# Kernel optimization log

Hardware: AMD Instinct MI355X
Metric: run time of the kernel (lower is better)

## Reference

```python
import jax, jax.numpy as jnp
import numpy as np

B, T, N, C = 16, 12, 2048, 64
WIN = 3                    # window_size
F = 3                      # len(filters) branches
NW = T - WIN + 1           # number of windows = 10


def setup_inputs() -> dict:
    key = jax.random.key(0)
    k0, k1, k2, k3, k4 = jax.random.split(key, 5)
    data = jax.random.normal(k0, (B, T, N, C), jnp.float32)
    # scale adj so aggregated features stay O(1)
    adj = jax.random.normal(k1, (WIN * N, WIN * N), jnp.float32) / np.float32(np.sqrt(WIN * N))
    temporal_emb = jax.random.normal(k2, (1, T, 1, C), jnp.float32) * 0.1
    spatial_emb = jax.random.normal(k3, (1, 1, N, C), jnp.float32) * 0.1
    # per-window, per-filter GLU linear: C -> 2C
    W = jax.random.normal(k4, (NW, F, C, 2 * C), jnp.float32) / np.float32(np.sqrt(C))
    b = jnp.zeros((NW, F, 2 * C), jnp.float32)
    return {"data": data, "adj": adj, "temporal_emb": temporal_emb,
            "spatial_emb": spatial_emb, "W": W, "b": b}


def reference(data, adj, temporal_emb, spatial_emb, W, b):
    # data: (B,T,N,C); adj: (3N,3N)
    x = data + temporal_emb + spatial_emb                     # (B,T,N,C)
    # sliding windows of 3 time steps, flattened to 3N nodes  # (B,NW,3N,C)
    wins = jnp.stack([x[:, i:i + WIN].reshape(B, WIN * N, C) for i in range(NW)], axis=1)
    # only the middle N rows of the bmm output survive the mid-step slice,
    # so aggregate with just those rows of adj (same math, less work)
    adj_mid = adj[(WIN - 1) // 2 * N:(WIN + 1) // 2 * N]      # (N, 3N)
    agg = jnp.einsum('mn,bwnc->bwmc', adj_mid, wins)          # (B,NW,N,C)
    # per-window per-filter linear C -> 2C, then GLU
    pre = jnp.einsum('bwnc,wfcd->bwfnd', agg, W) + b[None, :, :, None, :]  # (B,NW,F,N,2C)
    lhs, rhs = jnp.split(pre, 2, axis=-1)
    glu = lhs * jax.nn.sigmoid(rhs)                           # (B,NW,F,N,C)
    # max over filter branches -> (B, T-2, N, C)
    return jnp.max(glu, axis=2)
```

## Files before the change

kernel.cpp:

```cpp
#include <hip/hip_runtime.h>
#include <hip/hip_bf16.h>

#define B_ 16
#define T_ 12
#define N_ 2048
#define C_ 64
#define NW_ 10
#define K_ 6144

#define NT32 192
#define ALDS32 4096
#define BLDS32 10240

typedef __attribute__((ext_vector_type(8))) short bf16x8;
typedef __attribute__((ext_vector_type(4))) float f32x4;

__device__ __forceinline__ unsigned short f2bf(float f) {
  union { float f; unsigned int u; } v; v.f = f;
  unsigned int u = v.u;
  return (unsigned short)((u + 0x7FFFu + ((u >> 16) & 1u)) >> 16);
}

__device__ __forceinline__ void gload16(const void* g, void* l) {
  __builtin_amdgcn_global_load_lds(
      (const __attribute__((address_space(1))) unsigned int*)g,
      (__attribute__((address_space(3))) unsigned int*)l, 16, 0, 0);
}

template<int N>
__device__ __forceinline__ void vmw() {
  if constexpr (N == 5) asm volatile("s_waitcnt vmcnt(5)" ::: "memory");
  else                  asm volatile("s_waitcnt vmcnt(0)" ::: "memory");
}

__global__ __launch_bounds__(256) void prep_x2(const float* __restrict__ data,
                                               const float* __restrict__ temb,
                                               const float* __restrict__ semb,
                                               unsigned short* __restrict__ xbt2) {
  int idx = blockIdx.x * 256 + threadIdx.x;
  int q = idx & 511;
  int btnb = idx >> 9;
  int nb = btnb & 31;
  int bt = btnb >> 5;
  int t = bt % T_;
  int o = q >> 6, c = q & 63;
  int n0 = nb * 64 + o * 8;
  float te = temb[t * C_ + c];
  union { unsigned short s[8]; uint4 v; } pk;
#pragma unroll
  for (int e = 0; e < 8; ++e) {
    int n = n0 + e;
    float d = data[((size_t)bt * N_ + n) * C_ + c];
    float se = semb[(size_t)n * C_ + c];
    pk.s[e] = f2bf(d + te + se);
  }
  *(uint4*)(xbt2 + (size_t)idx * 8) = pk.v;
}

__global__ __launch_bounds__(256) void prep_adj3(const float* __restrict__ adj,
                                                 unsigned short* __restrict__ adjb3) {
  int idx = blockIdx.x * 256 + threadIdx.x;
  int s = idx & 63;
  int l4 = s >> 4, l15 = s & 15;
  int chunk = idx >> 6;
  int rg = chunk & 7;
  int KK = (chunk >> 3) & 1;
  int tb = chunk >> 4;
  int t = tb % 96;
  int bmt = tb / 96;
  int m = bmt * 128 + rg * 16 + l15;
  int k = t * 64 + KK * 32 + l4 * 8;
  const float* src = adj + ((size_t)(N_ + m)) * K_ + k;
  float4 a = *(const float4*)src;
  float4 b4 = *(const float4*)(src + 4);
  union { unsigned short s8[8]; uint4 v; } pk;
  pk.s8[0] = f2bf(a.x);  pk.s8[1] = f2bf(a.y);  pk.s8[2] = f2bf(a.z);  pk.s8[3] = f2bf(a.w);
  pk.s8[4] = f2bf(b4.x); pk.s8[5] = f2bf(b4.y); pk.s8[6] = f2bf(b4.z); pk.s8[7] = f2bf(b4.w);
  *(uint4*)(adjb3 + (size_t)idx * 8) = pk.v;
}

__global__ __launch_bounds__(256) void prep_w(const float* __restrict__ W,
                                              unsigned short* __restrict__ wbt) {
  int idx = blockIdx.x * 256 + threadIdx.x;
  int c = idx & 63;
  int d = (idx >> 6) & 127;
  int wf = idx >> 13;
  float v = W[((size_t)wf * 64 + c) * 128 + d];
  wbt[idx] = f2bf(v);
}

struct SegCtx {
  const unsigned short* Asrc;
  const unsigned short* Xroot;
  int lane, wid, wid5, l4, l15, fbase;
  int bconst[5];
};

template<int UA, int UB3>
__device__ __forceinline__ void phase32(const SegCtx& s, unsigned short* ldsA,
                                        unsigned short* ldsB, int u, f32x4 (&acc)[8][5]) {
  if (u + 1 < NT32) {
    const unsigned short* As = s.Asrc + (size_t)(u + 1) * 4096;
    unsigned short* Ad = ldsA + (UA ^ 1) * ALDS32;
#pragma unroll
    for (int ci = 0; ci < 2; ++ci) {
      int rg = s.wid * 2 + ci;
      gload16(As + rg * 512 + s.lane * 8, Ad + rg * 512);
    }
  }
  if (u + 2 < NT32) {
    const unsigned short* Bs = s.Xroot + (size_t)(u + 2) * 2048;
    unsigned short* Bd = ldsB + ((UB3 + 2) % 3) * BLDS32;
#pragma unroll
    for (int ci = 0; ci < 5; ++ci) {
      int cg = s.wid5 + ci;
      gload16(Bs + s.bconst[ci], Bd + cg * 512);
    }
  }
  const unsigned short* Ab = ldsA + UA * ALDS32;
  const unsigned short* Bb = ldsB + UB3 * BLDS32;
  bf16x8 af[8], bfv[5];
#pragma unroll
  for (int c = 0; c < 5; ++c)
    bfv[c] = *(const bf16x8*)(Bb + (s.wid5 + c) * 512 + s.fbase);
#pragma unroll
  for (int i = 0; i < 8; ++i)
    af[i] = *(const bf16x8*)(Ab + i * 512 + s.fbase);
  __builtin_amdgcn_s_setprio(1);
#pragma unroll
  for (int i = 0; i < 8; ++i)
#pragma unroll
    for (int c = 0; c < 5; ++c)
      acc[i][c] = __builtin_amdgcn_mfma_f32_16x16x32_bf16(af[i], bfv[c], acc[i][c], 0, 0, 0);
  __builtin_amdgcn_s_setprio(0);
  if (u < NT32 - 2) vmw<5>();
  else if (u == NT32 - 2) vmw<0>();
  if (u < NT32 - 1) {
    __builtin_amdgcn_s_barrier();
    __builtin_amdgcn_sched_barrier(0);
  }
}

__global__ __launch_bounds__(256, 2) void gemm_agg(const unsigned short* __restrict__ adjb3,
                                                   const unsigned short* __restrict__ xbt2,
                                                   unsigned short* __restrict__ aggb) {
  __shared__ __align__(16) unsigned short ldsA[2 * ALDS32];
  __shared__ __align__(16) unsigned short ldsB[3 * BLDS32];
  int bid = blockIdx.x;
  int bmt = bid & 15;
  int bs = bid >> 4;
  int b = bs >> 1;
  int w0 = (bs & 1) * 5;
  int tid = threadIdx.x;
  SegCtx s;
  s.lane = tid & 63; s.wid = tid >> 6;
  s.wid5 = s.wid * 5;
  s.l4 = s.lane >> 4; s.l15 = s.lane & 15;
  s.fbase = s.l4 * 128 + s.l15 * 8;
  s.Asrc = adjb3 + (size_t)bmt * 786432;
  s.Xroot = xbt2 + ((size_t)(b * T_ + w0)) * C_ * N_;
  int bOffLane = s.l4 * 512 + s.l15 * 8;
#pragma unroll
  for (int ci = 0; ci < 5; ++ci) {
    int cg = s.wid5 + ci;
    s.bconst[ci] = (cg >> 2) * 131072 + (cg & 3) * 128 + bOffLane;
  }

  f32x4 acc[8][5];
#pragma unroll
  for (int i = 0; i < 8; ++i)
#pragma unroll
    for (int c = 0; c < 5; ++c) acc[i][c] = (f32x4)0.f;

  __builtin_amdgcn_sched_barrier(0);
#pragma unroll
  for (int ci = 0; ci < 2; ++ci) {
    int rg = s.wid * 2 + ci;
    gload16(s.Asrc + rg * 512 + s.lane * 8, ldsA + rg * 512);
  }
#pragma unroll
  for (int ci = 0; ci < 5; ++ci)
    gload16(s.Xroot + s.bconst[ci], ldsB + (s.wid5 + ci) * 512);
#pragma unroll
  for (int ci = 0; ci < 5; ++ci)
    gload16(s.Xroot + 2048 + s.bconst[ci], ldsB + BLDS32 + (s.wid5 + ci) * 512);
  vmw<5>();
  __builtin_amdgcn_s_barrier();
  __builtin_amdgcn_sched_barrier(0);

  for (int it = 0; it < NT32 / 6; ++it) {
    int u = it * 6;
    phase32<0, 0>(s, ldsA, ldsB, u,     acc);
    phase32<1, 1>(s, ldsA, ldsB, u + 1, acc);
    phase32<0, 2>(s, ldsA, ldsB, u + 2, acc);
    phase32<1, 0>(s, ldsA, ldsB, u + 3, acc);
    phase32<0, 1>(s, ldsA, ldsB, u + 4, acc);
    phase32<1, 2>(s, ldsA, ldsB, u + 5, acc);
  }

  unsigned short* Ob0 = aggb + (size_t)(b * NW_ + w0) * N_ * C_;
#pragma unroll
  for (int c = 0; c < 5; ++c) {
    int col = s.wid * 80 + c * 16 + s.l15;
    int g = col >> 6, cc = col & 63;
    unsigned short* Ob = Ob0 + (size_t)g * N_ * C_ + cc;
#pragma unroll
    for (int i = 0; i < 8; ++i) {
      int n0 = bmt * 128 + i * 16 + s.l4 * 4;
#pragma unroll
      for (int q = 0; q < 4; ++q)
        Ob[(size_t)(n0 + q) * C_] = f2bf(acc[i][c][q]);
    }
  }
}

__global__ __launch_bounds__(256) void glu_out(const unsigned short* __restrict__ aggb,
                                               const unsigned short* __restrict__ wbt,
                                               const float* __restrict__ bias,
                                               float* __restrict__ out) {
  __shared__ __align__(16) unsigned short sW[3 * 128 * 64];
  int bn = blockIdx.x, bw = blockIdx.y;
  int w = bw % NW_;
  int tid = threadIdx.x, lane = tid & 63, wid = tid >> 6;
  int lrow8 = lane >> 3, jl = lane & 7;
  int l15 = lane & 15, l4 = lane >> 4;
  const unsigned short* Wsrc = wbt + (size_t)w * 3 * 128 * 64;
  for (int ci = 0; ci < 12; ++ci) {
    int chunk = wid * 12 + ci;
    int row = chunk * 8 + lrow8;
    int jg = jl ^ (row & 7);
    gload16(Wsrc + (size_t)row * 64 + jg * 8, &sW[chunk * 512]);
  }
  const unsigned short* Abase = aggb + ((size_t)bw * N_ + bn * 128 + wid * 32) * C_;
  bf16x8 af[2][2];
  for (int i = 0; i < 2; ++i)
    for (int kh = 0; kh < 2; ++kh)
      af[i][kh] = *(const bf16x8*)(Abase + (size_t)(i * 16 + l15) * C_ + kh * 32 + l4 * 8);
  __syncthreads();

  float omax[2][4][4];
  for (int i = 0; i < 2; ++i)
    for (int j = 0; j < 4; ++j)
      for (int r = 0; r < 4; ++r) omax[i][j][r] = -INFINITY;

  for (int f = 0; f < 3; ++f) {
    f32x4 acc[2][8];
    for (int i = 0; i < 2; ++i)
      for (int j = 0; j < 8; ++j) acc[i][j] = (f32x4)0.f;
    for (int kh = 0; kh < 2; ++kh) {
      int gchunk = kh * 4 + l4;
      for (int j = 0; j < 8; ++j) {
        int row = f * 128 + j * 16 + l15;
        int ch = gchunk ^ (row & 7);
        bf16x8 bfr = *(const bf16x8*)&sW[row * 64 + ch * 8];
        for (int i = 0; i < 2; ++i)
          acc[i][j] = __builtin_amdgcn_mfma_f32_16x16x32_bf16(af[i][kh], bfr, acc[i][j], 0, 0, 0);
      }
    }
    for (int j = 0; j < 4; ++j) {
      float bl = bias[(w * 3 + f) * 128 + j * 16 + l15];
      float br = bias[(w * 3 + f) * 128 + 64 + j * 16 + l15];
      for (int i = 0; i < 2; ++i)
        for (int r = 0; r < 4; ++r) {
          float lhs = acc[i][j][r] + bl;
          float rhs = acc[i][j + 4][r] + br;
          float g = lhs / (1.f + __expf(-rhs));
          omax[i][j][r] = fmaxf(omax[i][j][r], g);
        }
    }
  }
  float* Obase = out + ((size_t)bw * N_ + bn * 128 + wid * 32) * C_;
  for (int i = 0; i < 2; ++i)
    for (int j = 0; j < 4; ++j)
      for (int r = 0; r < 4; ++r)
        Obase[(size_t)(i * 16 + l4 * 4 + r) * C_ + j * 16 + l15] = omax[i][j][r];
}

extern "C" void kernel_launch(void* const* d_in, const int* in_sizes, int n_in,
                              void* d_out, int out_size, void* d_ws, size_t ws_size,
                              hipStream_t stream) {
  const float* data = (const float*)d_in[0];
  const float* adj  = (const float*)d_in[1];
  const float* temb = (const float*)d_in[2];
  const float* semb = (const float*)d_in[3];
  const float* W    = (const float*)d_in[4];
  const float* bias = (const float*)d_in[5];
  float* out = (float*)d_out;

  char* ws = (char*)d_ws;
  unsigned short* xbt2  = (unsigned short*)ws;
  unsigned short* adjb3 = (unsigned short*)(ws + 50331648);
  unsigned short* wbt   = (unsigned short*)(ws + 75497472);
  unsigned short* aggb  = (unsigned short*)(ws + 75988992);

  hipLaunchKernelGGL(prep_x2,   dim3(12288), dim3(256), 0, stream, data, temb, semb, xbt2);
  hipLaunchKernelGGL(prep_adj3, dim3(6144),  dim3(256), 0, stream, adj, adjb3);
  hipLaunchKernelGGL(prep_w,    dim3(960),   dim3(256), 0, stream, W, wbt);
  hipLaunchKernelGGL(gemm_agg,  dim3(512),   dim3(256), 0, stream, adjb3, xbt2, aggb);
  hipLaunchKernelGGL(glu_out,   dim3(16, 160), dim3(256), 0, stream, aggb, wbt, bias, out);
}
```

Before: 312.4 us.

## Load adjacency tiles straight into registers and drop per-step block barriers

The adjacency (A) operand of the aggregation GEMM is no longer staged through double-buffered LDS. Each wave now reads its A fragments from global memory directly into registers: the high half for the current step, the low half prefetched for the next step. Because every wave reads only the LDS region of X columns it loaded itself, the per-step s_barrier is removed and replaced with hand-tuned vmcnt waits. This removes LDS traffic and block-wide sync for A, but all four waves now fetch the same A tile redundantly, which raises global/L2 traffic, and the fixed vmcnt thresholds are fragile.

```diff
diff --git a/kernel.cpp b/kernel.cpp
--- a/kernel.cpp
+++ b/kernel.cpp
@@ -9,7 +9,6 @@
 #define K_ 6144
 
 #define NT32 192
-#define ALDS32 4096
 #define BLDS32 10240
 
 typedef __attribute__((ext_vector_type(8))) short bf16x8;
@@ -29,8 +28,11 @@
 
 template<int N>
 __device__ __forceinline__ void vmw() {
-  if constexpr (N == 5) asm volatile("s_waitcnt vmcnt(5)" ::: "memory");
-  else                  asm volatile("s_waitcnt vmcnt(0)" ::: "memory");
+  if constexpr (N == 30)      asm volatile("s_waitcnt vmcnt(30)" ::: "memory");
+  else if constexpr (N == 25) asm volatile("s_waitcnt vmcnt(25)" ::: "memory");
+  else if constexpr (N == 22) asm volatile("s_waitcnt vmcnt(22)" ::: "memory");
+  else if constexpr (N == 16) asm volatile("s_waitcnt vmcnt(16)" ::: "memory");
+  else                        asm volatile("s_waitcnt vmcnt(0)" ::: "memory");
 }
 
 __global__ __launch_bounds__(256) void prep_x2(const float* __restrict__ data,
@@ -92,59 +94,59 @@
 struct SegCtx {
   const unsigned short* Asrc;
   const unsigned short* Xroot;
-  int lane, wid, wid5, l4, l15, fbase;
+  int wid5, fbase;
   int bconst[5];
 };
 
-template<int UA, int UB3>
-__device__ __forceinline__ void phase32(const SegCtx& s, unsigned short* ldsA,
-                                        unsigned short* ldsB, int u, f32x4 (&acc)[8][5]) {
-  if (u + 1 < NT32) {
-    const unsigned short* As = s.Asrc + (size_t)(u + 1) * 4096;
-    unsigned short* Ad = ldsA + (UA ^ 1) * ALDS32;
-#pragma unroll
-    for (int ci = 0; ci < 2; ++ci) {
-      int rg = s.wid * 2 + ci;
-      gload16(As + rg * 512 + s.lane * 8, Ad + rg * 512);
-    }
-  }
+template<int U3>
+__device__ __forceinline__ void phase32(const SegCtx& s, unsigned short* ldsB, int u,
+                                        bf16x8 (&alo)[4], bf16x8 (&aloN)[4],
+                                        f32x4 (&acc)[8][5]) {
+  const unsigned short* Au = s.Asrc + (size_t)u * 4096;
+  bf16x8 ahi[4];
+#pragma unroll
+  for (int i = 0; i < 4; ++i)
+    ahi[i] = *(const bf16x8*)(Au + (4 + i) * 512 + s.fbase);
   if (u + 2 < NT32) {
     const unsigned short* Bs = s.Xroot + (size_t)(u + 2) * 2048;
-    unsigned short* Bd = ldsB + ((UB3 + 2) % 3) * BLDS32;
-#pragma unroll
-    for (int ci = 0; ci < 5; ++ci) {
-      int cg = s.wid5 + ci;
-      gload16(Bs + s.bconst[ci], Bd + cg * 512);
-    }
-  }
-  const unsigned short* Ab = ldsA + UA * ALDS32;
-  const unsigned short* Bb = ldsB + UB3 * BLDS32;
-  bf16x8 af[8], bfv[5];
+    unsigned short* Bd = ldsB + ((U3 + 2) % 3) * BLDS32;
+#pragma unroll
+    for (int ci = 0; ci < 5; ++ci)
+      gload16(Bs + s.bconst[ci], Bd + (s.wid5 + ci) * 512);
+  }
+  if (u + 1 < NT32) {
+    const unsigned short* An = Au + 4096;
+#pragma unroll
+    for (int i = 0; i < 4; ++i)
+      aloN[i] = *(const bf16x8*)(An + i * 512 + s.fbase);
+  }
+  if (u == 0) vmw<22>();
+  else if (u < NT32 - 2) vmw<30>();
+  else if (u == NT32 - 2) vmw<25>();
+  else vmw<16>();
+  const unsigned short* Bb = ldsB + U3 * BLDS32;
+  bf16x8 bfv[5];
 #pragma unroll
   for (int c = 0; c < 5; ++c)
     bfv[c] = *(const bf16x8*)(Bb + (s.wid5 + c) * 512 + s.fbase);
-#pragma unroll
-  for (int i = 0; i < 8; ++i)
-    af[i] = *(const bf16x8*)(Ab + i * 512 + s.fbase);
   __builtin_amdgcn_s_setprio(1);
 #pragma unroll
-  for (int i = 0; i < 8; ++i)
+  for (int i = 0; i < 4; ++i)
 #pragma unroll
     for (int c = 0; c < 5; ++c)
-      acc[i][c] = __builtin_amdgcn_mfma_f32_16x16x32_bf16(af[i], bfv[c], acc[i][c], 0, 0, 0);
+      acc[i][c] = __builtin_amdgcn_mfma_f32_16x16x32_bf16(alo[i], bfv[c], acc[i][c], 0, 0, 0);
+#pragma unroll
+  for (int i = 0; i < 4; ++i)
+#pragma unroll
+    for (int c = 0; c < 5; ++c)
+      acc[4 + i][c] = __builtin_amdgcn_mfma_f32_16x16x32_bf16(ahi[i], bfv[c], acc[4 + i][c], 0, 0, 0);
   __builtin_amdgcn_s_setprio(0);
-  if (u < NT32 - 2) vmw<5>();
-  else if (u == NT32 - 2) vmw<0>();
-  if (u < NT32 - 1) {
-    __builtin_amdgcn_s_barrier();
-    __builtin_amdgcn_sched_barrier(0);
-  }
+  __builtin_amdgcn_sched_barrier(0);
 }
 
 __global__ __launch_bounds__(256, 2) void gemm_agg(const unsigned short* __restrict__ adjb3,
                                                    const unsigned short* __restrict__ xbt2,
                                                    unsigned short* __restrict__ aggb) {
-  __shared__ __align__(16) unsigned short ldsA[2 * ALDS32];
   __shared__ __align__(16) unsigned short ldsB[3 * BLDS32];
   int bid = blockIdx.x;
   int bmt = bid & 15;
@@ -152,14 +154,14 @@
   int b = bs >> 1;
   int w0 = (bs & 1) * 5;
   int tid = threadIdx.x;
+  int lane = tid & 63, wid = tid >> 6;
+  int l4 = lane >> 4, l15 = lane & 15;
   SegCtx s;
-  s.lane = tid & 63; s.wid = tid >> 6;
-  s.wid5 = s.wid * 5;
-  s.l4 = s.lane >> 4; s.l15 = s.lane & 15;
-  s.fbase = s.l4 * 128 + s.l15 * 8;
+  s.wid5 = wid * 5;
+  s.fbase = l4 * 128 + l15 * 8;
   s.Asrc = adjb3 + (size_t)bmt * 786432;
   s.Xroot = xbt2 + ((size_t)(b * T_ + w0)) * C_ * N_;
-  int bOffLane = s.l4 * 512 + s.l15 * 8;
+  int bOffLane = l4 * 512 + l15 * 8;
 #pragma unroll
   for (int ci = 0; ci < 5; ++ci) {
     int cg = s.wid5 + ci;
@@ -172,41 +174,38 @@
 #pragma unroll
     for (int c = 0; c < 5; ++c) acc[i][c] = (f32x4)0.f;
 
+  bf16x8 P[4], Q[4];
   __builtin_amdgcn_sched_barrier(0);
-#pragma unroll
-  for (int ci = 0; ci < 2; ++ci) {
-    int rg = s.wid * 2 + ci;
-    gload16(s.Asrc + rg * 512 + s.lane * 8, ldsA + rg * 512);
-  }
 #pragma unroll
   for (int ci = 0; ci < 5; ++ci)
     gload16(s.Xroot + s.bconst[ci], ldsB + (s.wid5 + ci) * 512);
 #pragma unroll
   for (int ci = 0; ci < 5; ++ci)
     gload16(s.Xroot + 2048 + s.bconst[ci], ldsB + BLDS32 + (s.wid5 + ci) * 512);
-  vmw<5>();
-  __builtin_amdgcn_s_barrier();
+#pragma unroll
+  for (int i = 0; i < 4; ++i)
+    P[i] = *(const bf16x8*)(s.Asrc + i * 512 + s.fbase);
   __builtin_amdgcn_sched_barrier(0);
 
   for (int it = 0; it < NT32 / 6; ++it) {
     int u = it * 6;
-    phase32<0, 0>(s, ldsA, ldsB, u,     acc);
-    phase32<1, 1>(s, ldsA, ldsB, u + 1, acc);
-    phase32<0, 2>(s, ldsA, ldsB, u + 2, acc);
-    phase32<1, 0>(s, ldsA, ldsB, u + 3, acc);
-    phase32<0, 1>(s, ldsA, ldsB, u + 4, acc);
-    phase32<1, 2>(s, ldsA, ldsB, u + 5, acc);
+    phase32<0>(s, ldsB, u,     P, Q, acc);
+    phase32<1>(s, ldsB, u + 1, Q, P, acc);
+    phase32<2>(s, ldsB, u + 2, P, Q, acc);
+    phase32<0>(s, ldsB, u + 3, Q, P, acc);
+    phase32<1>(s, ldsB, u + 4, P, Q, acc);
+    phase32<2>(s, ldsB, u + 5, Q, P, acc);
   }
 
   unsigned short* Ob0 = aggb + (size_t)(b * NW_ + w0) * N_ * C_;
 #pragma unroll
   for (int c = 0; c < 5; ++c) {
-    int col = s.wid * 80 + c * 16 + s.l15;
+    int col = wid * 80 + c * 16 + l15;
     int g = col >> 6, cc = col & 63;
     unsigned short* Ob = Ob0 + (size_t)g * N_ * C_ + cc;
 #pragma unroll
     for (int i = 0; i < 8; ++i) {
-      int n0 = bmt * 128 + i * 16 + s.l4 * 4;
+      int n0 = bmt * 128 + i * 16 + l4 * 4;
 #pragma unroll
       for (int q = 0; q < 4; ++q)
         Ob[(size_t)(n0 + q) * C_] = f2bf(acc[i][c][q]);
```

Measured after the change: 863.2 us. 2.76x slower.

## Load B operand straight from global into registers instead of LDS

Applied to the files above, without the earlier changes.

The B tile (windowed features) is no longer staged through a triple-buffered LDS ring. Each wave now loads its own B fragments directly from global memory into double-buffered registers, one step ahead. This shrinks LDS use and removes the LDS write/read round trip for B. In exchange the prefetch distance drops from two steps to one, register pressure rises, and global load latency is more exposed each iteration.

```diff
diff --git a/kernel.cpp b/kernel.cpp
--- a/kernel.cpp
+++ b/kernel.cpp
@@ -9,8 +9,6 @@
 #define K_ 6144
 
 #define NT32 192
-#define ALDS32 4096
-#define BLDS32 10240
 
 typedef __attribute__((ext_vector_type(8))) short bf16x8;
 typedef __attribute__((ext_vector_type(4))) float f32x4;
@@ -92,37 +90,35 @@
 struct SegCtx {
   const unsigned short* Asrc;
   const unsigned short* Xroot;
-  int lane, wid, wid5, l4, l15, fbase;
+  int lane, wid, wid5, fbase;
   int bconst[5];
 };
 
-template<int UA, int UB3>
-__device__ __forceinline__ void phase32(const SegCtx& s, unsigned short* ldsA,
-                                        unsigned short* ldsB, int u, f32x4 (&acc)[8][5]) {
+__device__ __forceinline__ void stage_A(const SegCtx& s, unsigned short* ldsA, int u) {
+  const unsigned short* As = s.Asrc + (size_t)u * 4096;
+  unsigned short* Ad = ldsA + (u & 1) * 4096;
+#pragma unroll
+  for (int ci = 0; ci < 2; ++ci) {
+    int rg = s.wid * 2 + ci;
+    gload16(As + rg * 512 + s.lane * 8, Ad + rg * 512);
+  }
+}
+
+template<int UA>
+__device__ __forceinline__ void phase32(const SegCtx& s, unsigned short* ldsA, int u,
+                                        bf16x8 (&Bc)[5], bf16x8 (&Bn)[5],
+                                        f32x4 (&acc)[8][5]) {
   if (u + 1 < NT32) {
-    const unsigned short* As = s.Asrc + (size_t)(u + 1) * 4096;
-    unsigned short* Ad = ldsA + (UA ^ 1) * ALDS32;
-#pragma unroll
-    for (int ci = 0; ci < 2; ++ci) {
-      int rg = s.wid * 2 + ci;
-      gload16(As + rg * 512 + s.lane * 8, Ad + rg * 512);
-    }
-  }
-  if (u + 2 < NT32) {
-    const unsigned short* Bs = s.Xroot + (size_t)(u + 2) * 2048;
-    unsigned short* Bd = ldsB + ((UB3 + 2) % 3) * BLDS32;
-#pragma unroll
-    for (int ci = 0; ci < 5; ++ci) {
-      int cg = s.wid5 + ci;
-      gload16(Bs + s.bconst[ci], Bd + cg * 512);
-    }
-  }
-  const unsigned short* Ab = ldsA + UA * ALDS32;
-  const unsigned short* Bb = ldsB + UB3 * BLDS32;
-  bf16x8 af[8], bfv[5];
-#pragma unroll
-  for (int c = 0; c < 5; ++c)
-    bfv[c] = *(const bf16x8*)(Bb + (s.wid5 + c) * 512 + s.fbase);
+    stage_A(s, ldsA, u + 1);
+    __builtin_amdgcn_sched_barrier(0);
+    const unsigned short* Bs = s.Xroot + (size_t)(u + 1) * 2048;
+#pragma unroll
+    for (int ci = 0; ci < 5; ++ci)
+      Bn[ci] = *(const bf16x8*)(Bs + s.bconst[ci]);
+    __builtin_amdgcn_sched_barrier(0);
+  }
+  const unsigned short* Ab = ldsA + UA * 4096;
+  bf16x8 af[8];
 #pragma unroll
   for (int i = 0; i < 8; ++i)
     af[i] = *(const bf16x8*)(Ab + i * 512 + s.fbase);
@@ -131,11 +127,10 @@
   for (int i = 0; i < 8; ++i)
 #pragma unroll
     for (int c = 0; c < 5; ++c)
-      acc[i][c] = __builtin_amdgcn_mfma_f32_16x16x32_bf16(af[i], bfv[c], acc[i][c], 0, 0, 0);
+      acc[i][c] = __builtin_amdgcn_mfma_f32_16x16x32_bf16(af[i], Bc[c], acc[i][c], 0, 0, 0);
   __builtin_amdgcn_s_setprio(0);
-  if (u < NT32 - 2) vmw<5>();
-  else if (u == NT32 - 2) vmw<0>();
   if (u < NT32 - 1) {
+    vmw<5>();
     __builtin_amdgcn_s_barrier();
     __builtin_amdgcn_sched_barrier(0);
   }
@@ -144,22 +139,22 @@
 __global__ __launch_bounds__(256, 2) void gemm_agg(const unsigned short* __restrict__ adjb3,
                                                    const unsigned short* __restrict__ xbt2,
                                                    unsigned short* __restrict__ aggb) {
-  __shared__ __align__(16) unsigned short ldsA[2 * ALDS32];
-  __shared__ __align__(16) unsigned short ldsB[3 * BLDS32];
+  __shared__ __align__(16) unsigned short ldsA[2 * 4096];
   int bid = blockIdx.x;
   int bmt = bid & 15;
   int bs = bid >> 4;
   int b = bs >> 1;
   int w0 = (bs & 1) * 5;
   int tid = threadIdx.x;
+  int lane = tid & 63, wid = tid >> 6;
+  int l4 = lane >> 4, l15 = lane & 15;
   SegCtx s;
-  s.lane = tid & 63; s.wid = tid >> 6;
-  s.wid5 = s.wid * 5;
-  s.l4 = s.lane >> 4; s.l15 = s.lane & 15;
-  s.fbase = s.l4 * 128 + s.l15 * 8;
+  s.lane = lane; s.wid = wid;
+  s.wid5 = wid * 5;
+  s.fbase = l4 * 128 + l15 * 8;
   s.Asrc = adjb3 + (size_t)bmt * 786432;
   s.Xroot = xbt2 + ((size_t)(b * T_ + w0)) * C_ * N_;
-  int bOffLane = s.l4 * 512 + s.l15 * 8;
+  int bOffLane = l4 * 512 + l15 * 8;
 #pragma unroll
   for (int ci = 0; ci < 5; ++ci) {
     int cg = s.wid5 + ci;
@@ -172,41 +167,32 @@
 #pragma unroll
     for (int c = 0; c < 5; ++c) acc[i][c] = (f32x4)0.f;
 
-  __builtin_amdgcn_sched_barrier(0);
-#pragma unroll
-  for (int ci = 0; ci < 2; ++ci) {
-    int rg = s.wid * 2 + ci;
-    gload16(s.Asrc + rg * 512 + s.lane * 8, ldsA + rg * 512);
-  }
+  bf16x8 B0[5], B1[5];
+  __builtin_amdgcn_sched_barrier(0);
+  stage_A(s, ldsA, 0);
+  __builtin_amdgcn_sched_barrier(0);
 #pragma unroll
   for (int ci = 0; ci < 5; ++ci)
-    gload16(s.Xroot + s.bconst[ci], ldsB + (s.wid5 + ci) * 512);
-#pragma unroll
-  for (int ci = 0; ci < 5; ++ci)
-    gload16(s.Xroot + 2048 + s.bconst[ci], ldsB + BLDS32 + (s.wid5 + ci) * 512);
+    B0[ci] = *(const bf16x8*)(s.Xroot + s.bconst[ci]);
+  __builtin_amdgcn_sched_barrier(0);
   vmw<5>();
   __builtin_amdgcn_s_barrier();
   __builtin_amdgcn_sched_barrier(0);
 
-  for (int it = 0; it < NT32 / 6; ++it) {
-    int u = it * 6;
-    phase32<0, 0>(s, ldsA, ldsB, u,     acc);
-    phase32<1, 1>(s, ldsA, ldsB, u + 1, acc);
-    phase32<0, 2>(s, ldsA, ldsB, u + 2, acc);
-    phase32<1, 0>(s, ldsA, ldsB, u + 3, acc);
-    phase32<0, 1>(s, ldsA, ldsB, u + 4, acc);
-    phase32<1, 2>(s, ldsA, ldsB, u + 5, acc);
+  for (int u = 0; u < NT32; u += 2) {
+    phase32<0>(s, ldsA, u,     B0, B1, acc);
+    phase32<1>(s, ldsA, u + 1, B1, B0, acc);
   }
 
   unsigned short* Ob0 = aggb + (size_t)(b * NW_ + w0) * N_ * C_;
 #pragma unroll
   for (int c = 0; c < 5; ++c) {
-    int col = s.wid * 80 + c * 16 + s.l15;
+    int col = wid * 80 + c * 16 + l15;
     int g = col >> 6, cc = col & 63;
     unsigned short* Ob = Ob0 + (size_t)g * N_ * C_ + cc;
 #pragma unroll
     for (int i = 0; i < 8; ++i) {
-      int n0 = bmt * 128 + i * 16 + s.l4 * 4;
+      int n0 = bmt * 128 + i * 16 + l4 * 4;
 #pragma unroll
       for (int q = 0; q < 4; ++q)
         Ob[(size_t)(n0 + q) * C_] = f2bf(acc[i][c][q]);
```

New measurement: 322.6 us. +3.3%, slower.
